# Optimization experiments

Hardware: AMD Instinct MI355X
Metric: run time of the kernel (lower is better)

## Reference

```python
import jax, jax.numpy as jnp
import numpy as np

N = 30000          # num nodes
E = 480000         # num edges (avg degree 16)
K = 3              # Chebyshev filter order
IN = 128           # input feature dim
LAMBDA_MAX = 2.0   # PyG default spectral bound
DIMS = [IN, 16, 32, 64, 128, 256, 512]


def setup_inputs() -> dict:
    key = jax.random.key(0)
    ks = jax.random.split(key, 20)
    inp = {
        "x": jax.random.normal(ks[0], (N, IN), dtype=jnp.float32),
        "edge_index": jax.random.randint(ks[1], (2, E), 0, N, dtype=jnp.int32),
        "edge_weight": jax.random.uniform(ks[2], (E,), dtype=jnp.float32),
        "batch": jnp.arange(N, dtype=jnp.int32),  # each node its own graph -> pooling is identity
    }
    for i in range(6):
        fi, fo = DIMS[i], DIMS[i + 1]
        scale = 1.0 / np.sqrt(fi * K)
        inp[f"W{i+1}"] = jax.random.normal(ks[3 + 2 * i], (K, fi, fo), dtype=jnp.float32) * scale
        inp[f"b{i+1}"] = jnp.zeros((fo,), dtype=jnp.float32)
    inp["fc_w"] = jax.random.normal(ks[16], (512, 3), dtype=jnp.float32) * 0.05
    inp["fc_b"] = jnp.zeros((3,), dtype=jnp.float32)
    return inp


def _cheb_conv(x, row, col, w_off, diag, W, b):
    """ChebConv with rw-normalized, rescaled Laplacian Lhat = 2L/lmax - I.
    Lhat @ v = scatter(w_off * v[row] -> col) + diag * v."""
    def lmv(v):
        return jax.ops.segment_sum(w_off[:, None] * v[row], col, num_segments=N) + diag * v
    Tx0 = x
    out = Tx0 @ W[0]
    Tx1 = lmv(x)
    out = out + Tx1 @ W[1]
    for k in range(2, W.shape[0]):
        Tx2 = 2.0 * lmv(Tx1) - Tx0
        out = out + Tx2 @ W[k]
        Tx0, Tx1 = Tx1, Tx2
    return out + b


def _forward(x, edge_index, edge_weight, batch, Ws, bs, fc_w, fc_b):
    row, col = edge_index[0], edge_index[1]
    # random-walk Laplacian L = I - D^{-1} A, then Lhat = 2L/lmax - I
    deg = jax.ops.segment_sum(edge_weight, row, num_segments=N)
    deg_inv = jnp.where(deg > 0, 1.0 / deg, 0.0)
    w_off = -(2.0 / LAMBDA_MAX) * deg_inv[row] * edge_weight   # off-diagonal entries of Lhat
    diag = 2.0 / LAMBDA_MAX - 1.0                               # diagonal entry of Lhat (0 for lmax=2)
    h = x
    for W, b in zip(Ws, bs):
        h = _cheb_conv(h, row, col, w_off, diag, W, b)
        h = jax.ops.segment_max(h, batch, num_segments=N)  # global_max_pool; identity since batch=arange
        h = jax.nn.softplus(h)
    return h @ fc_w + fc_b


def reference(x, edge_index, edge_weight, batch, W1, b1, W2, b2, W3, b3, W4, b4, W5, b5, W6, b6, fc_w, fc_b):
    Ws = [W1, W2, W3, W4, W5, W6]
    bs = [b1, b2, b3, b4, b5, b6]
    return _forward(x, edge_index, edge_weight, batch, Ws, bs, fc_w, fc_b)
```

## Files before the change

kernel.cpp:

```cpp
#include <hip/hip_runtime.h>
#include <math.h>
#include <stdint.h>

#define NN 30000
#define EE 480000
#define MPAD 30080

typedef __attribute__((ext_vector_type(8))) short short8;
typedef __attribute__((ext_vector_type(4))) float floatx4;

__device__ __forceinline__ float b2f(ushort u) {
    union { uint u; float f; } c; c.u = ((uint)u) << 16; return c.f;
}
__device__ __forceinline__ ushort f2b(float f) {
    union { float f; uint u; } c; c.f = f;
    uint u = c.u;
    uint r = (u + 0x7FFFu + ((u >> 16) & 1u)) >> 16;
    return (ushort)r;
}
__device__ __forceinline__ float softplus_f(float x) {
    float a = fabsf(x) * 1.44269504f;
    float t = __builtin_amdgcn_exp2f(-a);
    float l = __builtin_amdgcn_logf(1.f + t);
    return fmaxf(x, 0.f) + 0.69314718f * l;
}

__device__ __forceinline__ void gld_lds16(const void* g, void* lds) {
    __builtin_amdgcn_global_load_lds(
        (__attribute__((address_space(1))) void*)(uintptr_t)(g),
        (__attribute__((address_space(3))) void*)(uint32_t)(uintptr_t)(lds),
        16, 0, 0);
}

__device__ __forceinline__ void barrier_raw() {
    __asm__ volatile("s_barrier" ::: "memory");
}
template <int N>
__device__ __forceinline__ void waitcnt_vm() {
    if constexpr (N == 0) __asm__ volatile("s_waitcnt vmcnt(0)" ::: "memory");
    else if constexpr (N == 2) __asm__ volatile("s_waitcnt vmcnt(2)" ::: "memory");
    else if constexpr (N == 3) __asm__ volatile("s_waitcnt vmcnt(3)" ::: "memory");
    else if constexpr (N == 4) __asm__ volatile("s_waitcnt vmcnt(4)" ::: "memory");
    else if constexpr (N == 8) __asm__ volatile("s_waitcnt vmcnt(8)" ::: "memory");
}


__global__ __launch_bounds__(256) void pre1_fused(
        const int* __restrict__ row, const int* __restrict__ col,
        const float* __restrict__ ew,
        float* __restrict__ deg, int* __restrict__ counts,
        const float* __restrict__ x, ushort* __restrict__ xb,
        const float* __restrict__ W1, const float* __restrict__ W2,
        const float* __restrict__ W3, const float* __restrict__ W4,
        const float* __restrict__ W5, const float* __restrict__ W6,
        ushort* __restrict__ B1, ushort* __restrict__ B2,
        ushort* __restrict__ B3, ushort* __restrict__ B4,
        ushort* __restrict__ B5, ushort* __restrict__ B6) {
    int b = blockIdx.x;
    int kind, id;
    if (b < 7500) {
        if ((b & 3) == 0) { kind = 0; id = b >> 2; }
        else { kind = 1; id = (b >> 2) * 3 + (b & 3) - 1; }
    } else { kind = 1; id = 5625 + (b - 7500); }
    if (kind == 0) {
        int e = id * 256 + threadIdx.x;
        atomicAdd(&deg[row[e]], ew[e]);
        atomicAdd(&counts[col[e]], 1);
    } else if (id < 3750) {
        int idx = id * 256 + threadIdx.x;
        float4 v = *(const float4*)(x + idx * 4);
        ushort4 o;
        o.x = f2b(v.x); o.y = f2b(v.y); o.z = f2b(v.z); o.w = f2b(v.w);
        *(ushort4*)(xb + idx * 4) = o;
    } else {
        int idx = (id - 3750) * 256 + threadIdx.x;
        if (idx < 6144) {
            int r = idx >> 7, k = idx & 127;
            int j = r >> 4, n = r & 15;
            B1[idx] = f2b(W1[(j * 128 + k) * 16 + n]);
        } else if (idx < 8192) {
            int t = idx - 6144; int n = t >> 6, k = t & 63;
            B2[t] = f2b(k < 48 ? W2[k * 32 + n] : 0.f);
        } else if (idx < 14336) {
            int t = idx - 8192; int n = t / 96, k = t - n * 96;
            B3[t] = f2b(W3[k * 64 + n]);
        } else if (idx < 38912) {
            int t = idx - 14336; int n = t / 192, k = t - n * 192;
            B4[t] = f2b(W4[k * 128 + n]);
        } else if (idx < 137216) {
            int t = idx - 38912; int n = t / 384, k = t - n * 384;
            B5[t] = f2b(W5[k * 256 + n]);
        } else if (idx < 530432) {
            int t = idx - 137216; int n = t / 768, k = t - n * 768;
            B6[t] = f2b(W6[k * 512 + n]);
        }
    }
}

__global__ __launch_bounds__(1024) void scan_one(
        const int* __restrict__ counts, int* __restrict__ offs,
        int* __restrict__ cursor) {
    __shared__ int ws[16];
    int t = threadIdx.x;
    int wave = t >> 6, lane = t & 63;
    int base = t * 32;
    int c[32];
    int s = 0;
    if (base < NN) {
        #pragma unroll
        for (int g = 0; g < 8; ++g) {
            int4 v = *(const int4*)(counts + base + g * 4);
            c[g * 4 + 0] = v.x; c[g * 4 + 1] = v.y;
            c[g * 4 + 2] = v.z; c[g * 4 + 3] = v.w;
        }
        #pragma unroll
        for (int i = 0; i < 32; ++i)
            if (base + i >= NN) c[i] = 0;
        #pragma unroll
        for (int i = 0; i < 32; ++i) s += c[i];
    } else {
        #pragma unroll
        for (int i = 0; i < 32; ++i) c[i] = 0;
    }
    int incl = s;
    #pragma unroll
    for (int off = 1; off < 64; off <<= 1) {
        int xv = __shfl_up(incl, off);
        if (lane >= off) incl += xv;
    }
    if (lane == 63) ws[wave] = incl;
    __syncthreads();
    if (wave == 0) {
        int v = (lane < 16) ? ws[lane] : 0;
        #pragma unroll
        for (int off = 1; off < 16; off <<= 1) {
            int xv = __shfl_up(v, off);
            if (lane >= off) v += xv;
        }
        if (lane < 16) ws[lane] = v;
    }
    __syncthreads();
    int wbase = (wave == 0) ? 0 : ws[wave - 1];
    int run = wbase + incl - s;
    if (base < NN) {
        int o[32];
        #pragma unroll
        for (int i = 0; i < 32; ++i) { o[i] = run; run += c[i]; }
        #pragma unroll
        for (int g = 0; g < 8; ++g) {
            int4 v = make_int4(o[g * 4], o[g * 4 + 1], o[g * 4 + 2], o[g * 4 + 3]);
            *(int4*)(offs + base + g * 4) = v;
            *(int4*)(cursor + base + g * 4) = v;
        }
    }
    if (t == 0) offs[NN] = EE;
}

template <int BN, bool ACT>
__device__ __forceinline__ void gemm_mfma_body(
        int bid, const ushort* __restrict__ A, int lda, int K,
        const ushort* __restrict__ Bt, const float* __restrict__ bias,
        ushort* __restrict__ Out, int ldo) {
    constexpr int BM = 128, BK = 32;
    constexpr int SM = 32;
    constexpr int FM = 2;
    constexpr int FN = BN / 16;
    constexpr int CB = BN / 16;
    constexpr int WAITN = (BN == 64) ? 3 : 2;
    __shared__ __align__(16) ushort As[2][BM][BK];
    __shared__ __align__(16) ushort Bs[2][BN][BK];
    int tid = threadIdx.x;
    int wv = tid >> 6, ln = tid & 63;
    int q = ln >> 4, r16 = ln & 15;
    int m0 = bid * BM;

    int lrow = ln >> 2;
    int gseg = (ln & 3) ^ ((ln >> 3) & 3);
    const ushort* Abase = A + (size_t)(m0 + lrow) * lda + gseg * 8;
    const ushort* Bbase = Bt + (size_t)lrow * K + gseg * 8;

    floatx4 acc[FM][FN];
    #pragma unroll
    for (int i = 0; i < FM; ++i)
        #pragma unroll
        for (int j = 0; j < FN; ++j) acc[i][j] = (floatx4){0.f, 0.f, 0.f, 0.f};

    int sw = (q ^ ((r16 >> 1) & 3)) * 8;
    int aoff[FM], boff[FN];
    #pragma unroll
    for (int i = 0; i < FM; ++i) aoff[i] = (wv * SM + i * 16 + r16) * BK + sw;
    #pragma unroll
    for (int j = 0; j < FN; ++j) boff[j] = (j * 16 + r16) * BK + sw;

    auto stage = [&](int b, int k0) {
        gld_lds16(Abase + (size_t)(wv * 16) * lda + k0, &As[b][wv * 16][0]);
        gld_lds16(Abase + (size_t)(64 + wv * 16) * lda + k0, &As[b][64 + wv * 16][0]);
        if constexpr (CB == 4) {
            gld_lds16(Bbase + (size_t)(wv * 16) * K + k0, &Bs[b][wv * 16][0]);
        } else {
            if (wv < CB) gld_lds16(Bbase + (size_t)(wv * 16) * K + k0, &Bs[b][wv * 16][0]);
        }
    };
    auto compute = [&](int b) {
        const ushort* ldsA = &As[b][0][0];
        const ushort* ldsB = &Bs[b][0][0];
        short8 af[FM], bf[FN];
        #pragma unroll
        for (int i = 0; i < FM; ++i) af[i] = *(const short8*)(ldsA + aoff[i]);
        #pragma unroll
        for (int j = 0; j < FN; ++j) bf[j] = *(const short8*)(ldsB + boff[j]);
        #pragma unroll
        for (int i = 0; i < FM; ++i)
            #pragma unroll
            for (int j = 0; j < FN; ++j)
                acc[i][j] = __builtin_amdgcn_mfma_f32_16x16x32_bf16(
                    af[i], bf[j], acc[i][j], 0, 0, 0);
    };

    int nIter = K / BK;
    stage(0, 0);
    for (int i = 0; i < nIter; ++i) {
        int cur = i & 1;
        barrier_raw();
        if (i + 1 < nIter) {
            stage(cur ^ 1, (i + 1) * BK);
            waitcnt_vm<WAITN>();
        } else {
            waitcnt_vm<0>();
        }
        barrier_raw();
        compute(cur);
    }
    #pragma unroll
    for (int i = 0; i < FM; ++i) {
        #pragma unroll
        for (int j = 0; j < FN; ++j) {
            int n = j * 16 + r16;
            float bv = ACT ? bias[n] : 0.f;
            #pragma unroll
            for (int r = 0; r < 4; ++r) {
                int m = m0 + wv * SM + i * 16 + q * 4 + r;
                float v = acc[i][j][r] + bv;
                Out[(size_t)m * ldo + n] = f2b(ACT ? softplus_f(v) : v);
            }
        }
    }
}

template <int BN, bool ACT = true>
__global__ __launch_bounds__(256) void gemm_mfma(
        const ushort* __restrict__ A, int lda, int K,
        const ushort* __restrict__ Bt,
        const float* __restrict__ bias,
        ushort* __restrict__ Out, int ldo) {
    gemm_mfma_body<BN, ACT>(blockIdx.x, A, lda, K, Bt, bias, Out, ldo);
}

__global__ __launch_bounds__(256) void pre2_fused(
        const int* __restrict__ row, const int* __restrict__ col,
        const float* __restrict__ ew, const float* __restrict__ deg,
        int* __restrict__ cursor, int2* __restrict__ csr_rw,
        const ushort* __restrict__ xb, const ushort* __restrict__ Bt1,
        ushort* __restrict__ Ybuf) {
    int b = blockIdx.x;
    if (b < MPAD / 128) {
        gemm_mfma_body<48, false>(b, xb, 128, 128, Bt1, nullptr, Ybuf, 48);
    } else {
        int e = (b - MPAD / 128) * 256 + threadIdx.x;
        int r = row[e];
        float d = deg[r];
        float wv = (d > 0.f) ? (-ew[e] / d) : 0.f;
        int pos = atomicAdd(&cursor[col[e]], 1);
        csr_rw[pos] = make_int2(r, __float_as_int(wv));
    }
}

template <int FI>
__global__ __launch_bounds__(256) void lmv_bf16(
        const ushort* __restrict__ A, ushort* __restrict__ Out,
        const ushort* __restrict__ Sub, int ldi, int ldo,
        const int* __restrict__ offs, const int2* __restrict__ rw,
        float scale, int N) {
    constexpr int NPW = 64 / FI;
    int wave = threadIdx.x >> 6;
    int lane = threadIdx.x & 63;
    int sub = lane / FI;
    int fbase = lane & (FI - 1);
    int node = blockIdx.x * (4 * NPW) + wave * NPW + sub;
    if (node >= N) return;
    int e0 = offs[node], e1 = offs[node + 1];
    float acc[4];
    #pragma unroll
    for (int c = 0; c < 4; ++c) acc[c] = 0.f;
    int e = e0;
    for (; e + 4 <= e1; e += 4) {
        int2 u0 = rw[e], u1 = rw[e + 1], u2 = rw[e + 2], u3 = rw[e + 3];
        acc[0] += __int_as_float(u0.y) * b2f(A[(size_t)u0.x * ldi + fbase]);
        acc[1] += __int_as_float(u1.y) * b2f(A[(size_t)u1.x * ldi + fbase]);
        acc[2] += __int_as_float(u2.y) * b2f(A[(size_t)u2.x * ldi + fbase]);
        acc[3] += __int_as_float(u3.y) * b2f(A[(size_t)u3.x * ldi + fbase]);
    }
    for (; e < e1; ++e) {
        int2 u = rw[e];
        acc[0] += __int_as_float(u.y) * b2f(A[(size_t)u.x * ldi + fbase]);
    }
    float a = (acc[0] + acc[1]) + (acc[2] + acc[3]);
    ushort* o = Out + (size_t)node * ldo + fbase;
    if (Sub) {
        const ushort* s = Sub + (size_t)node * ldo + fbase;
        *o = f2b(scale * a - b2f(*s));
    } else {
        *o = f2b(scale * a);
    }
}

__global__ __launch_bounds__(256) void lmv_l1_final(
        const ushort* __restrict__ Z,
        const ushort* __restrict__ Y,
        const float* __restrict__ b,
        ushort* __restrict__ Out,
        const int* __restrict__ offs, const int2* __restrict__ rw, int N) {
    int wave = threadIdx.x >> 6;
    int lane = threadIdx.x & 63;
    int sub = lane >> 4, f = lane & 15;
    int node = blockIdx.x * 16 + wave * 4 + sub;
    if (node >= N) return;
    int e0 = offs[node], e1 = offs[node + 1];
    const ushort* Z2 = Z + 16;
    float acc[4];
    #pragma unroll
    for (int c = 0; c < 4; ++c) acc[c] = 0.f;
    int e = e0;
    for (; e + 4 <= e1; e += 4) {
        int2 u0 = rw[e], u1 = rw[e + 1], u2 = rw[e + 2], u3 = rw[e + 3];
        acc[0] += __int_as_float(u0.y) * b2f(Z2[(size_t)u0.x * 32 + f]);
        acc[1] += __int_as_float(u1.y) * b2f(Z2[(size_t)u1.x * 32 + f]);
        acc[2] += __int_as_float(u2.y) * b2f(Z2[(size_t)u2.x * 32 + f]);
        acc[3] += __int_as_float(u3.y) * b2f(Z2[(size_t)u3.x * 32 + f]);
    }
    for (; e < e1; ++e) {
        int2 u = rw[e];
        acc[0] += __int_as_float(u.y) * b2f(Z2[(size_t)u.x * 32 + f]);
    }
    float z3 = (acc[0] + acc[1]) + (acc[2] + acc[3]);
    float y0 = b2f(Y[(size_t)node * 48 + f]);
    float y2 = b2f(Y[(size_t)node * 48 + 32 + f]);
    float z1 = b2f(Z[(size_t)node * 32 + f]);
    float v = y0 + z1 + 2.f * z3 - y2 + b[f];
    Out[(size_t)node * 64 + f] = f2b(softplus_f(v));
}

template <int VEC>
__global__ __launch_bounds__(256) void lmv_vec(
        const ushort* __restrict__ A, ushort* __restrict__ Out,
        const ushort* __restrict__ Sub, int ld,
        const int* __restrict__ offs, const int2* __restrict__ rw,
        float scale) {
    constexpr int CH = 8;
    int node = blockIdx.x * 4 + (threadIdx.x >> 6);
    int lane = threadIdx.x & 63;
    int fbase = lane * VEC;
    int e0 = __builtin_amdgcn_readfirstlane(offs[node]);
    int e1 = __builtin_amdgcn_readfirstlane(offs[node + 1]);
    float acc[CH][VEC];
    #pragma unroll
    for (int c = 0; c < CH; ++c)
        #pragma unroll
        for (int v = 0; v < VEC; ++v) acc[c][v] = 0.f;
    int e = e0;
    for (; e + CH <= e1; e += CH) {
        #pragma unroll
        for (int c = 0; c < CH; ++c) {
            int2 u = rw[e + c];
            int r = u.x;
            float we = __int_as_float(u.y);
            const ushort* pr = A + (size_t)r * ld + fbase;
            if constexpr (VEC == 4) {
                ushort4 uu = *(const ushort4*)pr;
                acc[c][0] += we * b2f(uu.x); acc[c][1] += we * b2f(uu.y);
                acc[c][2] += we * b2f(uu.z); acc[c][3] += we * b2f(uu.w);
            } else if constexpr (VEC == 2) {
                ushort2 uu = *(const ushort2*)pr;
                acc[c][0] += we * b2f(uu.x); acc[c][1] += we * b2f(uu.y);
            } else {
                acc[c][0] += we * b2f(*pr);
            }
        }
    }
    for (; e < e1; ++e) {
        int c = e & (CH - 1);
        int2 u = rw[e];
        int r = u.x;
        float we = __int_as_float(u.y);
        const ushort* pr = A + (size_t)r * ld + fbase;
        if constexpr (VEC == 4) {
            ushort4 uu = *(const ushort4*)pr;
            acc[c][0] += we * b2f(uu.x); acc[c][1] += we * b2f(uu.y);
            acc[c][2] += we * b2f(uu.z); acc[c][3] += we * b2f(uu.w);
        } else if constexpr (VEC == 2) {
            ushort2 uu = *(const ushort2*)pr;
            acc[c][0] += we * b2f(uu.x); acc[c][1] += we * b2f(uu.y);
        } else {
            acc[c][0] += we * b2f(*pr);
        }
    }
    #pragma unroll
    for (int c = 1; c < CH; ++c)
        #pragma unroll
        for (int v = 0; v < VEC; ++v) acc[0][v] += acc[c][v];
    ushort* o = Out + (size_t)node * ld + fbase;
    if (Sub) {
        const ushort* s = Sub + (size_t)node * ld + fbase;
        ushort tmp[VEC];
        #pragma unroll
        for (int v = 0; v < VEC; ++v) tmp[v] = f2b(scale * acc[0][v] - b2f(s[v]));
        #pragma unroll
        for (int v = 0; v < VEC; ++v) o[v] = tmp[v];
    } else {
        #pragma unroll
        for (int v = 0; v < VEC; ++v) o[v] = f2b(scale * acc[0][v]);
    }
}

template <bool FC = false, int YB = 0>
__global__ __launch_bounds__(256) void gemm_bk64(
        const ushort* __restrict__ A, int lda, int K,
        const ushort* __restrict__ Bt,
        const float* __restrict__ bias,
        ushort* __restrict__ Out, int ldo,
        const float* __restrict__ fcw, float* __restrict__ fcout) {
    constexpr int BM = 128, BN = 128, BK = 64;
    __shared__ __align__(16) ushort As[2][BM][BK];
    __shared__ __align__(16) ushort Bs[2][BN][BK];
    int tid = threadIdx.x;
    int wv = tid >> 6, ln = tid & 63;
    int wm = wv & 1, wn = wv >> 1;
    int q = ln >> 4, r16 = ln & 15;
    int nwg = gridDim.x;
    int orig = blockIdx.x;
    int xcd = orig & 7;
    int qq = nwg >> 3, rr = nwg & 7;
    int wbase = (xcd < rr) ? xcd * (qq + 1) : rr * (qq + 1) + (xcd - rr) * qq;
    int wgid = wbase + (orig >> 3);
    int yb = wgid & ((1 << YB) - 1);
    int xb = wgid >> YB;
    int m0 = xb * BM;
    int n0 = yb * BN;

    int lrow8 = ln >> 3, slds = ln & 7;
    int gseg = slds ^ lrow8;
    const ushort* Abase = A + (size_t)(m0 + lrow8) * lda + gseg * 8;
    const ushort* Bbase = Bt + (size_t)(n0 + lrow8) * K + gseg * 8;

    floatx4 acc[4][4];
    #pragma unroll
    for (int i = 0; i < 4; ++i)
        #pragma unroll
        for (int j = 0; j < 4; ++j) acc[i][j] = (floatx4){0.f, 0.f, 0.f, 0.f};

    int r7 = r16 & 7;
    int aoff[2][4], boff[2][4];
    #pragma unroll
    for (int s = 0; s < 2; ++s) {
        int segp = ((s * 4 + q) ^ r7) * 8;
        #pragma unroll
        for (int i = 0; i < 4; ++i) {
            aoff[s][i] = (wm * 64 + i * 16 + r16) * BK + segp;
            boff[s][i] = (wn * 64 + i * 16 + r16) * BK + segp;
        }
    }

    auto stage = [&](int b, int k0) {
        #pragma unroll
        for (int g = 0; g < 4; ++g)
            gld_lds16(Abase + (size_t)(wv * 8 + g * 32) * lda + k0,
                      &As[b][wv * 8 + g * 32][0]);
        #pragma unroll
        for (int g = 0; g < 4; ++g)
            gld_lds16(Bbase + (size_t)(wv * 8 + g * 32) * K + k0,
                      &Bs[b][wv * 8 + g * 32][0]);
    };
    auto compute = [&](int b) {
        const ushort* ldsA = &As[b][0][0];
        const ushort* ldsB = &Bs[b][0][0];
        #pragma unroll
        for (int s = 0; s < 2; ++s) {
            short8 af[4], bf[4];
            #pragma unroll
            for (int i = 0; i < 4; ++i) af[i] = *(const short8*)(ldsA + aoff[s][i]);
            #pragma unroll
            for (int j = 0; j < 4; ++j) bf[j] = *(const short8*)(ldsB + boff[s][j]);
            #pragma unroll
            for (int i = 0; i < 4; ++i)
                #pragma unroll
                for (int j = 0; j < 4; ++j)
                    acc[i][j] = __builtin_amdgcn_mfma_f32_16x16x32_bf16(
                        af[i], bf[j], acc[i][j], 0, 0, 0);
        }
    };

    int nIter = K / BK;
    stage(0, 0);
    for (int i = 0; i < nIter; ++i) {
        int cur = i & 1;
        barrier_raw();
        if (i + 1 < nIter) {
            stage(cur ^ 1, (i + 1) * BK);
            waitcnt_vm<8>();
        } else {
            waitcnt_vm<0>();
        }
        barrier_raw();
        compute(cur);
    }

    if constexpr (FC) {
        int pb = yb * 2 + wn;
        #pragma unroll
        for (int i = 0; i < 4; ++i) {
            #pragma unroll
            for (int r = 0; r < 4; ++r) {
                float p0 = 0.f, p1 = 0.f, p2 = 0.f;
                #pragma unroll
                for (int j = 0; j < 4; ++j) {
                    int n = n0 + wn * 64 + j * 16 + r16;
                    float v = softplus_f(acc[i][j][r] + bias[n]);
                    p0 += v * fcw[n * 3 + 0];
                    p1 += v * fcw[n * 3 + 1];
                    p2 += v * fcw[n * 3 + 2];
                }
                #pragma unroll
                for (int off = 1; off < 16; off <<= 1) {
                    p0 += __shfl_xor(p0, off);
                    p1 += __shfl_xor(p1, off);
                    p2 += __shfl_xor(p2, off);
                }
                if (r16 == 0) {
                    int m = m0 + wm * 64 + i * 16 + q * 4 + r;
                    float* dst = fcout + ((size_t)pb * MPAD + m) * 3;
                    dst[0] = p0; dst[1] = p1; dst[2] = p2;
                }
            }
        }
    } else {
        #pragma unroll
        for (int i = 0; i < 4; ++i) {
            #pragma unroll
            for (int j = 0; j < 4; ++j) {
                int n = n0 + wn * 64 + j * 16 + r16;
                float bv = bias[n];
                #pragma unroll
                for (int r = 0; r < 4; ++r) {
                    int m = m0 + wm * 64 + i * 16 + q * 4 + r;
                    Out[(size_t)m * ldo + n] = f2b(softplus_f(acc[i][j][r] + bv));
                }
            }
        }
    }
}

__global__ __launch_bounds__(256) void fc_reduce(
        const float* __restrict__ part, const float* __restrict__ fcb,
        float* __restrict__ out) {
    int idx = blockIdx.x * blockDim.x + threadIdx.x;
    if (idx >= NN * 3) return;
    int c = idx - (idx / 3) * 3;
    float s = 0.f;
    #pragma unroll
    for (int pb = 0; pb < 8; ++pb)
        s += part[(size_t)pb * MPAD * 3 + idx];
    out[idx] = s + fcb[c];
}

static inline size_t align256(size_t x) { return (x + 255) & ~(size_t)255; }

extern "C" void kernel_launch(void* const* d_in, const int* in_sizes, int n_in,
                              void* d_out, int out_size, void* d_ws, size_t ws_size,
                              hipStream_t stream) {
    const float* x   = (const float*)d_in[0];
    const int*   ei  = (const int*)d_in[1];
    const float* ew  = (const float*)d_in[2];
    const float* W[6]  = { (const float*)d_in[4],  (const float*)d_in[6],
                           (const float*)d_in[8],  (const float*)d_in[10],
                           (const float*)d_in[12], (const float*)d_in[14] };
    const float* Bv[6] = { (const float*)d_in[5],  (const float*)d_in[7],
                           (const float*)d_in[9],  (const float*)d_in[11],
                           (const float*)d_in[13], (const float*)d_in[15] };
    const float* fc_w = (const float*)d_in[16];
    const float* fc_b = (const float*)d_in[17];
    float* out = (float*)d_out;

    const int* e_row = ei;
    const int* e_col = ei + EE;

    const int fi_arr[5]   = { 16, 32, 64, 128, 256 };
    const int fo_arr[5]   = { 32, 64, 128, 256, 512 };
    const int Kpad_arr[5] = { 64, 96, 192, 384, 768 };
    const int ldo_arr[5]  = { 96, 192, 384, 768, 512 };

    char* p = (char*)d_ws;
    float* deg    = (float*)p; p += align256((size_t)NN * 4);
    int*   counts = (int*)p;   p += align256((size_t)NN * 4);
    int*   offs   = (int*)p;   p += align256((size_t)(NN + 1) * 4);
    int*   cursor = (int*)p;   p += align256((size_t)NN * 4);
    int2*  csr_rw = (int2*)p;  p += align256((size_t)EE * 8);
    ushort* Bt1   = (ushort*)p; p += align256((size_t)48 * 128 * 2);
    ushort* Bt[5];
    for (int L = 0; L < 5; ++L) {
        Bt[L] = (ushort*)p;
        p += align256((size_t)fo_arr[L] * Kpad_arr[L] * 2);
    }
    float* fcpart = (float*)p; p += align256((size_t)8 * MPAD * 3 * 4);
    ushort* xb   = (ushort*)p; p += align256((size_t)MPAD * 128 * 2);
    ushort* Ybuf = (ushort*)p; p += align256((size_t)MPAD * 48 * 2);
    ushort* Zbuf = (ushort*)p; p += align256((size_t)MPAD * 32 * 2);
    ushort* buf0 = (ushort*)p; p += align256((size_t)MPAD * 768 * 2);
    ushort* buf1 = (ushort*)p; p += align256((size_t)MPAD * 768 * 2);
    (void)ws_size; (void)n_in; (void)in_sizes; (void)out_size;

    hipMemsetAsync(deg, 0, align256((size_t)NN * 4) + (size_t)NN * 4, stream);

    pre1_fused<<<7697, 256, 0, stream>>>(
        e_row, e_col, ew, deg, counts, x, xb,
        W[0], W[1], W[2], W[3], W[4], W[5],
        Bt1, Bt[0], Bt[1], Bt[2], Bt[3], Bt[4]);

    scan_one<<<1, 1024, 0, stream>>>(counts, offs, cursor);

    pre2_fused<<<MPAD / 128 + EE / 256, 256, 0, stream>>>(
        e_row, e_col, ew, deg, cursor, csr_rw, xb, Bt1, Ybuf);

    lmv_bf16<32><<<(NN + 7) / 8, 256, 0, stream>>>(
        Ybuf + 16, Zbuf, nullptr, 48, 32, offs, csr_rw, 1.0f, NN);
    lmv_l1_final<<<(NN + 15) / 16, 256, 0, stream>>>(
        Zbuf, Ybuf, Bv[0], buf1, offs, csr_rw, NN);

    ushort* Abuf[5] = { buf1, buf0, buf1, buf0, buf1 };
    ushort* Obuf[5] = { buf0, buf1, buf0, buf1, buf0 };

    for (int L = 0; L < 5; ++L) {
        int fi = fi_arr[L];
        int ldA = Kpad_arr[L];
        int ldO = ldo_arr[L];
        ushort* A = Abuf[L];
        ushort* O = Obuf[L];

        switch (fi) {
            case 16:
                lmv_bf16<16><<<(NN + 15) / 16, 256, 0, stream>>>(
                    A, A + fi, nullptr, ldA, ldA, offs, csr_rw, 1.0f, NN);
                lmv_bf16<16><<<(NN + 15) / 16, 256, 0, stream>>>(
                    A + fi, A + 2 * fi, A, ldA, ldA, offs, csr_rw, 2.0f, NN);
                break;
            case 32:
                lmv_bf16<32><<<(NN + 7) / 8, 256, 0, stream>>>(
                    A, A + fi, nullptr, ldA, ldA, offs, csr_rw, 1.0f, NN);
                lmv_bf16<32><<<(NN + 7) / 8, 256, 0, stream>>>(
                    A + fi, A + 2 * fi, A, ldA, ldA, offs, csr_rw, 2.0f, NN);
                break;
            case 64:
                lmv_vec<1><<<NN / 4, 256, 0, stream>>>(
                    A, A + fi, nullptr, ldA, offs, csr_rw, 1.0f);
                lmv_vec<1><<<NN / 4, 256, 0, stream>>>(
                    A + fi, A + 2 * fi, A, ldA, offs, csr_rw, 2.0f);
                break;
            case 128:
                lmv_vec<2><<<NN / 4, 256, 0, stream>>>(
                    A, A + fi, nullptr, ldA, offs, csr_rw, 1.0f);
                lmv_vec<2><<<NN / 4, 256, 0, stream>>>(
                    A + fi, A + 2 * fi, A, ldA, offs, csr_rw, 2.0f);
                break;
            default:
                lmv_vec<4><<<NN / 4, 256, 0, stream>>>(
                    A, A + fi, nullptr, ldA, offs, csr_rw, 1.0f);
                lmv_vec<4><<<NN / 4, 256, 0, stream>>>(
                    A + fi, A + 2 * fi, A, ldA, offs, csr_rw, 2.0f);
                break;
        }

        int K = Kpad_arr[L];
        switch (fo_arr[L]) {
            case 32:
                gemm_mfma<32><<<dim3(MPAD / 128), 256, 0, stream>>>(
                    A, ldA, K, Bt[L], Bv[L + 1], O, ldO);
                break;
            case 64:
                gemm_mfma<64><<<dim3(MPAD / 128), 256, 0, stream>>>(
                    A, ldA, K, Bt[L], Bv[L + 1], O, ldO);
                break;
            case 128:
                gemm_bk64<false, 0><<<dim3(MPAD / 128), 256, 0, stream>>>(
                    A, ldA, K, Bt[L], Bv[L + 1], O, ldO, nullptr, nullptr);
                break;
            case 256:
                gemm_bk64<false, 1><<<dim3(MPAD / 128 * 2), 256, 0, stream>>>(
                    A, ldA, K, Bt[L], Bv[L + 1], O, ldO, nullptr, nullptr);
                break;
            default:
                gemm_bk64<true, 2><<<dim3(MPAD / 128 * 4), 256, 0, stream>>>(
                    A, ldA, K, Bt[L], Bv[L + 1], nullptr, 0, fc_w, fcpart);
                break;
        }
    }

    fc_reduce<<<(NN * 3 + 255) / 256, 256, 0, stream>>>(fcpart, fc_b, out);
}
```

Measured before the change: 463.8 us.

## Build CSR via per-block LDS histograms instead of global atomics

Degree and in-count accumulation now use 32 blocks, each keeping a shared-memory histogram over a chunk of edges and writing it out as a partial. A new column-reduce kernel sums the partials and turns the counts into per-block prefix offsets. The CSR fill then uses LDS cursors per block instead of global atomic cursors, and the memset is dropped. This removes contended global atomics, but only 32 blocks do the edge work, which may underuse the GPU and adds an extra kernel launch plus partial-buffer traffic.

```diff
diff --git a/kernel.cpp b/kernel.cpp
--- a/kernel.cpp
+++ b/kernel.cpp
@@ -5,6 +5,9 @@
 #define NN 30000
 #define EE 480000
 #define MPAD 30080
+#define NPAD 30720
+#define NB_HIST 32
+#define CHUNK 15000
 
 typedef __attribute__((ext_vector_type(8))) short short8;
 typedef __attribute__((ext_vector_type(4))) float floatx4;
@@ -48,7 +51,7 @@
 __global__ __launch_bounds__(256) void pre1_fused(
         const int* __restrict__ row, const int* __restrict__ col,
         const float* __restrict__ ew,
-        float* __restrict__ deg, int* __restrict__ counts,
+        int* __restrict__ Hpart, float* __restrict__ Dpart,
         const float* __restrict__ x, ushort* __restrict__ xb,
         const float* __restrict__ W1, const float* __restrict__ W2,
         const float* __restrict__ W3, const float* __restrict__ W4,
@@ -56,50 +59,114 @@
         ushort* __restrict__ B1, ushort* __restrict__ B2,
         ushort* __restrict__ B3, ushort* __restrict__ B4,
         ushort* __restrict__ B5, ushort* __restrict__ B6) {
+    __shared__ int hist[NPAD];
     int b = blockIdx.x;
-    int kind, id;
-    if (b < 7500) {
-        if ((b & 3) == 0) { kind = 0; id = b >> 2; }
-        else { kind = 1; id = (b >> 2) * 3 + (b & 3) - 1; }
-    } else { kind = 1; id = 5625 + (b - 7500); }
-    if (kind == 0) {
-        int e = id * 256 + threadIdx.x;
-        atomicAdd(&deg[row[e]], ew[e]);
-        atomicAdd(&counts[col[e]], 1);
-    } else if (id < 3750) {
-        int idx = id * 256 + threadIdx.x;
-        float4 v = *(const float4*)(x + idx * 4);
-        ushort4 o;
-        o.x = f2b(v.x); o.y = f2b(v.y); o.z = f2b(v.z); o.w = f2b(v.w);
-        *(ushort4*)(xb + idx * 4) = o;
+    int t = threadIdx.x;
+    if (b < NB_HIST) {
+        int e0 = b * CHUNK, e1 = e0 + CHUNK;
+        #pragma unroll
+        for (int i = 0; i < NPAD / 1024; ++i)
+            *(int4*)(&hist[(i * 256 + t) * 4]) = make_int4(0, 0, 0, 0);
+        __syncthreads();
+        int e = e0 + t;
+        for (; e + 2048 <= e1; e += 2048) {
+            int c0 = col[e],        c1 = col[e + 256];
+            int c2 = col[e + 512],  c3 = col[e + 768];
+            int c4 = col[e + 1024], c5 = col[e + 1280];
+            int c6 = col[e + 1536], c7 = col[e + 1792];
+            atomicAdd(&hist[c0], 1); atomicAdd(&hist[c1], 1);
+            atomicAdd(&hist[c2], 1); atomicAdd(&hist[c3], 1);
+            atomicAdd(&hist[c4], 1); atomicAdd(&hist[c5], 1);
+            atomicAdd(&hist[c6], 1); atomicAdd(&hist[c7], 1);
+        }
+        for (; e < e1; e += 256) atomicAdd(&hist[col[e]], 1);
+        __syncthreads();
+        #pragma unroll
+        for (int i = 0; i < NPAD / 1024; ++i)
+            *(int4*)(&Hpart[(size_t)b * NPAD + (i * 256 + t) * 4]) =
+                *(const int4*)(&hist[(i * 256 + t) * 4]);
+        __syncthreads();
+        float* histf = (float*)hist;
+        #pragma unroll
+        for (int i = 0; i < NPAD / 1024; ++i)
+            *(float4*)(&histf[(i * 256 + t) * 4]) = make_float4(0.f, 0.f, 0.f, 0.f);
+        __syncthreads();
+        e = e0 + t;
+        for (; e + 1024 <= e1; e += 1024) {
+            int r0 = row[e],       r1 = row[e + 256];
+            int r2 = row[e + 512], r3 = row[e + 768];
+            float w0 = ew[e],       w1 = ew[e + 256];
+            float w2 = ew[e + 512], w3 = ew[e + 768];
+            atomicAdd(&histf[r0], w0); atomicAdd(&histf[r1], w1);
+            atomicAdd(&histf[r2], w2); atomicAdd(&histf[r3], w3);
+        }
+        for (; e < e1; e += 256) atomicAdd(&histf[row[e]], ew[e]);
+        __syncthreads();
+        #pragma unroll
+        for (int i = 0; i < NPAD / 1024; ++i)
+            *(float4*)(&Dpart[(size_t)b * NPAD + (i * 256 + t) * 4]) =
+                *(const float4*)(&histf[(i * 256 + t) * 4]);
+    } else if (b < NB_HIST + 480) {
+        int id = b - NB_HIST;
+        #pragma unroll
+        for (int i = 0; i < 8; ++i) {
+            int idx = id * 2048 + i * 256 + t;
+            if (idx < NN * 128 / 4) {
+                float4 v = *(const float4*)(x + (size_t)idx * 4);
+                ushort4 o;
+                o.x = f2b(v.x); o.y = f2b(v.y); o.z = f2b(v.z); o.w = f2b(v.w);
+                *(ushort4*)(xb + (size_t)idx * 4) = o;
+            }
+        }
     } else {
-        int idx = (id - 3750) * 256 + threadIdx.x;
-        if (idx < 6144) {
-            int r = idx >> 7, k = idx & 127;
-            int j = r >> 4, n = r & 15;
-            B1[idx] = f2b(W1[(j * 128 + k) * 16 + n]);
-        } else if (idx < 8192) {
-            int t = idx - 6144; int n = t >> 6, k = t & 63;
-            B2[t] = f2b(k < 48 ? W2[k * 32 + n] : 0.f);
-        } else if (idx < 14336) {
-            int t = idx - 8192; int n = t / 96, k = t - n * 96;
-            B3[t] = f2b(W3[k * 64 + n]);
-        } else if (idx < 38912) {
-            int t = idx - 14336; int n = t / 192, k = t - n * 192;
-            B4[t] = f2b(W4[k * 128 + n]);
-        } else if (idx < 137216) {
-            int t = idx - 38912; int n = t / 384, k = t - n * 384;
-            B5[t] = f2b(W5[k * 256 + n]);
-        } else if (idx < 530432) {
-            int t = idx - 137216; int n = t / 768, k = t - n * 768;
-            B6[t] = f2b(W6[k * 512 + n]);
-        }
-    }
+        int id = b - NB_HIST - 480;
+        #pragma unroll
+        for (int i = 0; i < 8; ++i) {
+            int idx = id * 2048 + i * 256 + t;
+            if (idx < 6144) {
+                int r = idx >> 7, k = idx & 127;
+                int j = r >> 4, n = r & 15;
+                B1[idx] = f2b(W1[(j * 128 + k) * 16 + n]);
+            } else if (idx < 8192) {
+                int tt = idx - 6144; int n = tt >> 6, k = tt & 63;
+                B2[tt] = f2b(k < 48 ? W2[k * 32 + n] : 0.f);
+            } else if (idx < 14336) {
+                int tt = idx - 8192; int n = tt / 96, k = tt - n * 96;
+                B3[tt] = f2b(W3[k * 64 + n]);
+            } else if (idx < 38912) {
+                int tt = idx - 14336; int n = tt / 192, k = tt - n * 192;
+                B4[tt] = f2b(W4[k * 128 + n]);
+            } else if (idx < 137216) {
+                int tt = idx - 38912; int n = tt / 384, k = tt - n * 384;
+                B5[tt] = f2b(W5[k * 256 + n]);
+            } else if (idx < 530432) {
+                int tt = idx - 137216; int n = tt / 768, k = tt - n * 768;
+                B6[tt] = f2b(W6[k * 512 + n]);
+            }
+        }
+    }
+}
+
+__global__ __launch_bounds__(256) void col_reduce(
+        int* __restrict__ Hpart, const float* __restrict__ Dpart,
+        int* __restrict__ counts, float* __restrict__ deg) {
+    int c = blockIdx.x * 256 + threadIdx.x;
+    int run = 0;
+    #pragma unroll
+    for (int b = 0; b < NB_HIST; ++b) {
+        int v = Hpart[(size_t)b * NPAD + c];
+        Hpart[(size_t)b * NPAD + c] = run;
+        run += v;
+    }
+    counts[c] = run;
+    float s = 0.f;
+    #pragma unroll
+    for (int b = 0; b < NB_HIST; ++b) s += Dpart[(size_t)b * NPAD + c];
+    deg[c] = s;
 }
 
 __global__ __launch_bounds__(1024) void scan_one(
-        const int* __restrict__ counts, int* __restrict__ offs,
-        int* __restrict__ cursor) {
+        const int* __restrict__ counts, int* __restrict__ offs) {
     __shared__ int ws[16];
     int t = threadIdx.x;
     int wave = t >> 6, lane = t & 63;
@@ -114,9 +181,6 @@
             c[g * 4 + 2] = v.z; c[g * 4 + 3] = v.w;
         }
         #pragma unroll
-        for (int i = 0; i < 32; ++i)
-            if (base + i >= NN) c[i] = 0;
-        #pragma unroll
         for (int i = 0; i < 32; ++i) s += c[i];
     } else {
         #pragma unroll
@@ -150,7 +214,6 @@
         for (int g = 0; g < 8; ++g) {
             int4 v = make_int4(o[g * 4], o[g * 4 + 1], o[g * 4 + 2], o[g * 4 + 3]);
             *(int4*)(offs + base + g * 4) = v;
-            *(int4*)(cursor + base + g * 4) = v;
         }
     }
     if (t == 0) offs[NN] = EE;
@@ -259,19 +322,58 @@
 __global__ __launch_bounds__(256) void pre2_fused(
         const int* __restrict__ row, const int* __restrict__ col,
         const float* __restrict__ ew, const float* __restrict__ deg,
-        int* __restrict__ cursor, int2* __restrict__ csr_rw,
+        const int* __restrict__ offs, const int* __restrict__ Hpart,
+        int2* __restrict__ csr_rw,
         const ushort* __restrict__ xb, const ushort* __restrict__ Bt1,
         ushort* __restrict__ Ybuf) {
     int b = blockIdx.x;
-    if (b < MPAD / 128) {
-        gemm_mfma_body<48, false>(b, xb, 128, 128, Bt1, nullptr, Ybuf, 48);
+    if (b < NB_HIST) {
+        __shared__ int cur[NPAD];
+        int t = threadIdx.x;
+        #pragma unroll
+        for (int i = 0; i < NPAD / 1024; ++i) {
+            int idx = (i * 256 + t) * 4;
+            int4 o = *(const int4*)(offs + idx);
+            int4 pfx = *(const int4*)(Hpart + (size_t)b * NPAD + idx);
+            cur[idx + 0] = o.x + pfx.x;
+            cur[idx + 1] = o.y + pfx.y;
+            cur[idx + 2] = o.z + pfx.z;
+            cur[idx + 3] = o.w + pfx.w;
+        }
+        __syncthreads();
+        int e0 = b * CHUNK, e1 = e0 + CHUNK;
+        int e = e0 + t;
+        for (; e + 1024 <= e1; e += 1024) {
+            int r0 = row[e],       r1 = row[e + 256];
+            int r2 = row[e + 512], r3 = row[e + 768];
+            int c0 = col[e],       c1 = col[e + 256];
+            int c2 = col[e + 512], c3 = col[e + 768];
+            float w0 = ew[e],       w1 = ew[e + 256];
+            float w2 = ew[e + 512], w3 = ew[e + 768];
+            float d0 = deg[r0], d1 = deg[r1], d2 = deg[r2], d3 = deg[r3];
+            float v0 = (d0 > 0.f) ? (-w0 / d0) : 0.f;
+            float v1 = (d1 > 0.f) ? (-w1 / d1) : 0.f;
+            float v2 = (d2 > 0.f) ? (-w2 / d2) : 0.f;
+            float v3 = (d3 > 0.f) ? (-w3 / d3) : 0.f;
+            int p0 = atomicAdd(&cur[c0], 1);
+            int p1 = atomicAdd(&cur[c1], 1);
+            int p2 = atomicAdd(&cur[c2], 1);
+            int p3 = atomicAdd(&cur[c3], 1);
+            csr_rw[p0] = make_int2(r0, __float_as_int(v0));
+            csr_rw[p1] = make_int2(r1, __float_as_int(v1));
+            csr_rw[p2] = make_int2(r2, __float_as_int(v2));
+            csr_rw[p3] = make_int2(r3, __float_as_int(v3));
+        }
+        for (; e < e1; e += 256) {
+            int r = row[e];
+            float d = deg[r];
+            float wv = (d > 0.f) ? (-ew[e] / d) : 0.f;
+            int pos = atomicAdd(&cur[col[e]], 1);
+            csr_rw[pos] = make_int2(r, __float_as_int(wv));
+        }
     } else {
-        int e = (b - MPAD / 128) * 256 + threadIdx.x;
-        int r = row[e];
-        float d = deg[r];
-        float wv = (d > 0.f) ? (-ew[e] / d) : 0.f;
-        int pos = atomicAdd(&cursor[col[e]], 1);
-        csr_rw[pos] = make_int2(r, __float_as_int(wv));
+        gemm_mfma_body<48, false>(b - NB_HIST, xb, 128, 128, Bt1, nullptr,
+                                  Ybuf, 48);
     }
 }
 
@@ -599,10 +701,11 @@
     const int ldo_arr[5]  = { 96, 192, 384, 768, 512 };
 
     char* p = (char*)d_ws;
-    float* deg    = (float*)p; p += align256((size_t)NN * 4);
-    int*   counts = (int*)p;   p += align256((size_t)NN * 4);
-    int*   offs   = (int*)p;   p += align256((size_t)(NN + 1) * 4);
-    int*   cursor = (int*)p;   p += align256((size_t)NN * 4);
+    float* deg    = (float*)p; p += align256((size_t)NPAD * 4);
+    int*   counts = (int*)p;   p += align256((size_t)NPAD * 4);
+    int*   offs   = (int*)p;   p += align256((size_t)(NPAD + 4) * 4);
+    int*   Hpart  = (int*)p;   p += align256((size_t)NB_HIST * NPAD * 4);
+    float* Dpart  = (float*)p; p += align256((size_t)NB_HIST * NPAD * 4);
     int2*  csr_rw = (int2*)p;  p += align256((size_t)EE * 8);
     ushort* Bt1   = (ushort*)p; p += align256((size_t)48 * 128 * 2);
     ushort* Bt[5];
@@ -618,17 +721,18 @@
     ushort* buf1 = (ushort*)p; p += align256((size_t)MPAD * 768 * 2);
     (void)ws_size; (void)n_in; (void)in_sizes; (void)out_size;
 
-    hipMemsetAsync(deg, 0, align256((size_t)NN * 4) + (size_t)NN * 4, stream);
-
-    pre1_fused<<<7697, 256, 0, stream>>>(
-        e_row, e_col, ew, deg, counts, x, xb,
+
+    pre1_fused<<<NB_HIST + 480 + 260, 256, 0, stream>>>(
+        e_row, e_col, ew, Hpart, Dpart, x, xb,
         W[0], W[1], W[2], W[3], W[4], W[5],
         Bt1, Bt[0], Bt[1], Bt[2], Bt[3], Bt[4]);
 
-    scan_one<<<1, 1024, 0, stream>>>(counts, offs, cursor);
-
-    pre2_fused<<<MPAD / 128 + EE / 256, 256, 0, stream>>>(
-        e_row, e_col, ew, deg, cursor, csr_rw, xb, Bt1, Ybuf);
+    col_reduce<<<NPAD / 256, 256, 0, stream>>>(Hpart, Dpart, counts, deg);
+
+    scan_one<<<1, 1024, 0, stream>>>(counts, offs);
+
+    pre2_fused<<<NB_HIST + MPAD / 128, 256, 0, stream>>>(
+        e_row, e_col, ew, deg, offs, Hpart, csr_rw, xb, Bt1, Ybuf);
 
     lmv_bf16<32><<<(NN + 7) / 8, 256, 0, stream>>>(
         Ybuf + 16, Zbuf, nullptr, 48, 32, offs, csr_rw, 1.0f, NN);
```

New measurement: 459.7 us. Within noise of the previous version (-0.9%).
